# Kernel optimization log

Hardware: AMD Instinct MI355X
Metric: run time of the kernel (lower is better)

## Reference

```python
import jax, jax.numpy as jnp
import numpy as np

N, E, IN_DIM, HID, L = 50000, 800000, 64, 64, 3
EDGE_DIM = 2 * HID + 2  # src_h | dst_h | edge_feat


def setup_inputs() -> dict:
    key = jax.random.key(0)
    ks = jax.random.split(key, 32)
    s = 0.05
    inp = {
        "h": jax.random.normal(ks[0], (N, IN_DIM), jnp.float32),
        "e": jax.random.normal(ks[1], (E, 2), jnp.float32),
        "src": jax.random.randint(ks[2], (E,), 0, N),
        "dst": jax.random.randint(ks[3], (E,), 0, N),
        # input embedding
        "emb_W": jax.random.normal(ks[4], (IN_DIM, HID), jnp.float32) * s,
        "emb_b": jnp.zeros((HID,), jnp.float32),
        # per-GIN-layer params (stacked over L)
        "eps": jnp.zeros((L,), jnp.float32),  # learn_eps init 0
        "mlp_W1": jax.random.normal(ks[5], (L, HID, HID), jnp.float32) * s,
        "mlp_b1": jnp.zeros((L, HID), jnp.float32),
        "mlp_bn_s": jnp.ones((L, HID), jnp.float32),   # eval-mode BN folded: x*s+sh
        "mlp_bn_sh": jnp.zeros((L, HID), jnp.float32),
        "mlp_W2": jax.random.normal(ks[6], (L, HID, HID), jnp.float32) * s,
        "mlp_b2": jnp.zeros((L, HID), jnp.float32),
        "apply_bn_s": jnp.ones((L, HID), jnp.float32),
        "apply_bn_sh": jnp.zeros((L, HID), jnp.float32),
        "gin_bn_s": jnp.ones((L, HID), jnp.float32),
        "gin_bn_sh": jnp.zeros((L, HID), jnp.float32),
        # prediction heads (L+1 of them)
        "pred_W1": jax.random.normal(ks[7], (L + 1, EDGE_DIM, HID), jnp.float32) * s,
        "pred_b1": jnp.zeros((L + 1, HID), jnp.float32),
        "pred_W2": jax.random.normal(ks[8], (L + 1, HID, 1), jnp.float32) * s,
        "pred_b2": jnp.zeros((L + 1, 1), jnp.float32),
    }
    return inp


def reference(h, e, src, dst, emb_W, emb_b, eps,
              mlp_W1, mlp_b1, mlp_bn_s, mlp_bn_sh, mlp_W2, mlp_b2,
              apply_bn_s, apply_bn_sh, gin_bn_s, gin_bn_sh,
              pred_W1, pred_b1, pred_W2, pred_b2):
    n = h.shape[0]
    bn = lambda x, sc, sh: x * sc + sh  # eval-mode batchnorm (folded scale/shift)

    h = h @ emb_W + emb_b  # [N, HID]

    def edge_feat(hh):
        # gather node features onto edges: [E, 2*HID+2]
        return jnp.concatenate([hh[src], hh[dst], e], axis=1)

    def pred(ef, i):
        z = jax.nn.relu(ef @ pred_W1[i] + pred_b1[i])
        return z @ pred_W2[i] + pred_b2[i]  # [E, 1]

    score = pred(edge_feat(h), 0)
    for i in range(L):
        h_in = h
        # GIN sum aggregation: copy src features, sum at dst
        neigh = jax.ops.segment_sum(h[src], dst, num_segments=n)
        x = (1.0 + eps[i]) * h + neigh
        # MLP: Linear -> BN -> ReLU -> Linear
        x = jax.nn.relu(bn(x @ mlp_W1[i] + mlp_b1[i], mlp_bn_s[i], mlp_bn_sh[i]))
        x = x @ mlp_W2[i] + mlp_b2[i]
        # ApplyNodeFunc: BN -> ReLU
        x = jax.nn.relu(bn(x, apply_bn_s[i], apply_bn_sh[i]))
        # GINLayer post: BN -> ReLU -> residual (dropout=0 in eval)
        x = jax.nn.relu(bn(x, gin_bn_s[i], gin_bn_sh[i]))
        h = h_in + x
        score = score + pred(edge_feat(h), i + 1)
    return jax.nn.relu(score)
```

## Files before the change

### kernel.cpp

```cpp
#include <hip/hip_runtime.h>

typedef unsigned short ushort_t;
typedef unsigned int uint_t;

static __device__ __forceinline__ ushort_t f2bf(float f) {
    uint_t u = __float_as_uint(f);
    uint_t r = (u + 0x7FFFu + ((u >> 16) & 1u)) >> 16;
    return (ushort_t)r;
}
static __device__ __forceinline__ float bf2f(ushort_t u) {
    return __uint_as_float(((uint_t)u) << 16);
}
static __device__ __forceinline__ float bf2f_lo(uint_t u) {
    return __uint_as_float(u << 16);
}
static __device__ __forceinline__ float bf2f_hi(uint_t u) {
    return __uint_as_float(u & 0xffff0000u);
}
static __device__ __forceinline__ uint_t pack2(float lo, float hi) {
    return (uint_t)f2bf(lo) | ((uint_t)f2bf(hi) << 16);
}

static __device__ __forceinline__ float edge_p2(
    uint_t ax, uint_t ay, float4 brow, float ex, float ey,
    float4 wc0, float4 wc1, float4 w2v)
{
    float z0 = bf2f_lo(ax) + brow.x + ex*wc0.x + ey*wc1.x; z0 = fmaxf(z0, 0.f);
    float z1 = bf2f_hi(ax) + brow.y + ex*wc0.y + ey*wc1.y; z1 = fmaxf(z1, 0.f);
    float z2 = bf2f_lo(ay) + brow.z + ex*wc0.z + ey*wc1.z; z2 = fmaxf(z2, 0.f);
    float z3 = bf2f_hi(ay) + brow.w + ex*wc0.w + ey*wc1.w; z3 = fmaxf(z3, 0.f);
    return z0*w2v.x + z1*w2v.y + z2*w2v.z + z3*w2v.w;
}

#define RED16(p) { p += __shfl_xor(p,1); p += __shfl_xor(p,2); \
                   p += __shfl_xor(p,4); p += __shfl_xor(p,8); }

__global__ __launch_bounds__(256) void k_count(
    const int* __restrict__ dst, int* __restrict__ deg, int E)
{
    int e = blockIdx.x * 256 + threadIdx.x;
    if (e < E) atomicAdd(&deg[dst[e]], 1);
}

__global__ __launch_bounds__(1024) void k_scanA(
    const int* __restrict__ deg, int* __restrict__ partial,
    int* __restrict__ bsum, int N)
{
    __shared__ int wsum[16];
    int tid = threadIdx.x, lane = tid & 63, wid = tid >> 6;
    int idx = blockIdx.x * 1024 + tid;
    int v = (idx < N) ? deg[idx] : 0;
    int x = v;
#pragma unroll
    for (int o = 1; o < 64; o <<= 1) {
        int t = __shfl_up(x, o, 64);
        if (lane >= o) x += t;
    }
    if (lane == 63) wsum[wid] = x;
    __syncthreads();
    if (wid == 0) {
        int s = (lane < 16) ? wsum[lane] : 0;
#pragma unroll
        for (int o = 1; o < 16; o <<= 1) {
            int t = __shfl_up(s, o, 64);
            if (lane >= o) s += t;
        }
        if (lane < 16) wsum[lane] = s;
    }
    __syncthreads();
    int woff = (wid > 0) ? wsum[wid - 1] : 0;
    if (idx < N) partial[idx] = woff + x - v;
    if (tid == 0) bsum[blockIdx.x] = wsum[15];
}

__global__ __launch_bounds__(256) void k_scanB(
    int* __restrict__ bsum, int nb, int* __restrict__ totalp)
{
    __shared__ int s[256];
    int tid = threadIdx.x;
    int v = (tid < nb) ? bsum[tid] : 0;
    s[tid] = v;
    __syncthreads();
#pragma unroll
    for (int off = 1; off < 256; off <<= 1) {
        int t = (tid >= off) ? s[tid - off] : 0;
        __syncthreads();
        s[tid] += t;
        __syncthreads();
    }
    if (tid < nb) bsum[tid] = s[tid] - v;
    if (tid == 0) totalp[0] = s[255];
}

__global__ __launch_bounds__(256) void k_scanC(
    int* __restrict__ offsets, const int* __restrict__ bsum,
    int* __restrict__ cursor, int N)
{
    int idx = blockIdx.x * 256 + threadIdx.x;
    if (idx >= N) return;
    int o = offsets[idx] + bsum[idx >> 10];
    offsets[idx] = o;
    cursor[idx] = o;
}

__global__ __launch_bounds__(256) void k_fill(
    const int* __restrict__ src, const int* __restrict__ dst,
    const float* __restrict__ ep, int* __restrict__ cursor,
    int4* __restrict__ entries, int E)
{
    int ei = blockIdx.x * 256 + threadIdx.x;
    if (ei >= E) return;
    int pos = atomicAdd(&cursor[dst[ei]], 1);
    float2 ev = *(const float2*)(ep + 2 * (size_t)ei);
    entries[pos] = make_int4(src[ei], ei, __float_as_int(ev.x), __float_as_int(ev.y));
}

static __device__ __forceinline__ int deg_bucket(int d) {
    return d >= 63 ? 0 : (63 - d);
}

__global__ __launch_bounds__(256) void k_bcount(
    const int* __restrict__ offsets, int* __restrict__ bcnt, int N)
{
    __shared__ int hist[64];
    int tid = threadIdx.x;
    if (tid < 64) hist[tid] = 0;
    __syncthreads();
    int idx = blockIdx.x * 256 + tid;
    if (idx < N) {
        int d = offsets[idx + 1] - offsets[idx];
        atomicAdd(&hist[deg_bucket(d)], 1);
    }
    __syncthreads();
    if (tid < 64 && hist[tid]) atomicAdd(&bcnt[tid], hist[tid]);
}

__global__ __launch_bounds__(64) void k_bscan(
    int* __restrict__ bcnt, int* __restrict__ bcur)
{
    int lane = threadIdx.x;
    int v = bcnt[lane];
    int x = v;
#pragma unroll
    for (int o = 1; o < 64; o <<= 1) {
        int t = __shfl_up(x, o, 64);
        if (lane >= o) x += t;
    }
    bcur[lane] = x - v;
}

__global__ __launch_bounds__(256) void k_bfill(
    const int* __restrict__ offsets, int* __restrict__ bcur,
    int* __restrict__ perm, int N)
{
    __shared__ int hist[64];
    __shared__ int lbase[64];
    int tid = threadIdx.x;
    if (tid < 64) hist[tid] = 0;
    __syncthreads();
    int idx = blockIdx.x * 256 + tid;
    int b = 0, rank = 0;
    bool valid = (idx < N);
    if (valid) {
        int d = offsets[idx + 1] - offsets[idx];
        b = deg_bucket(d);
        rank = atomicAdd(&hist[b], 1);
    }
    __syncthreads();
    if (tid < 64) lbase[tid] = hist[tid] ? atomicAdd(&bcur[tid], hist[tid]) : 0;
    __syncthreads();
    if (valid) perm[lbase[b] + rank] = idx;
}

template <int WRITE>
static __device__ __forceinline__ void epi_tables16(
    float (*xs)[68], int row16, int li, int r, float4 o,
    const float* __restrict__ WAn, const float* __restrict__ bAn,
    const float* __restrict__ WBn,
    ushort_t* __restrict__ tab_out, ushort_t* __restrict__ B_out)
{
    xs[row16][4*li+0] = o.x; xs[row16][4*li+1] = o.y;
    xs[row16][4*li+2] = o.z; xs[row16][4*li+3] = o.w;
    float4 aA = *(const float4*)(bAn + 4 * li);
    float4 aB = make_float4(0.f, 0.f, 0.f, 0.f);
#pragma unroll
    for (int k = 0; k < 64; k++) {
        float xk = xs[row16][k];
        float4 wa = *(const float4*)(WAn + k * 64 + 4 * li);
        float4 wb = *(const float4*)(WBn + k * 64 + 4 * li);
        aA.x += xk * wa.x; aA.y += xk * wa.y; aA.z += xk * wa.z; aA.w += xk * wa.w;
        aB.x += xk * wb.x; aB.y += xk * wb.y; aB.z += xk * wb.z; aB.w += xk * wb.w;
    }
    if (WRITE == 1) {
        int4 cw;
        cw.x = (int)pack2(aA.x, aA.y);
        cw.y = (int)pack2(aA.z, aA.w);
        cw.z = (int)pack2(o.x, o.y);
        cw.w = (int)pack2(o.z, o.w);
        *(int4*)(tab_out + (size_t)r * 128 + li * 8) = cw;
    } else {
        ushort4 oa;
        oa.x = f2bf(aA.x); oa.y = f2bf(aA.y); oa.z = f2bf(aA.z); oa.w = f2bf(aA.w);
        *(ushort4*)(tab_out + (size_t)r * 64 + 4 * li) = oa;
    }
    ushort4 ob;
    ob.x = f2bf(aB.x); ob.y = f2bf(aB.y); ob.z = f2bf(aB.z); ob.w = f2bf(aB.w);
    *(ushort4*)(B_out + (size_t)r * 64 + 4 * li) = ob;
}

__global__ __launch_bounds__(256) void k_embed_ab(
    const float* __restrict__ in, const float* __restrict__ W,
    const float* __restrict__ bias, float* __restrict__ hout,
    const float* __restrict__ WA, const float* __restrict__ bA,
    const float* __restrict__ WB,
    ushort_t* __restrict__ comb_out, ushort_t* __restrict__ B_out, int N)
{
    __shared__ float xs[16][68];
    const int row16 = threadIdx.x >> 4;
    const int li    = threadIdx.x & 15;
    const int r     = blockIdx.x * 16 + row16;
    if (r >= N) return;
    float4 x4 = *(const float4*)(in + (size_t)r * 64 + 4 * li);
    xs[row16][4*li+0] = x4.x; xs[row16][4*li+1] = x4.y;
    xs[row16][4*li+2] = x4.z; xs[row16][4*li+3] = x4.w;
    float4 acc = *(const float4*)(bias + 4 * li);
#pragma unroll
    for (int k = 0; k < 64; k++) {
        float xk = xs[row16][k];
        float4 wv = *(const float4*)(W + k * 64 + 4 * li);
        acc.x += xk * wv.x; acc.y += xk * wv.y;
        acc.z += xk * wv.z; acc.w += xk * wv.w;
    }
    *(float4*)(hout + (size_t)r * 64 + 4 * li) = acc;
    epi_tables16<1>(xs, row16, li, r, acc, WA, bA, WB, comb_out, B_out);
}

__global__ __launch_bounds__(256) void k_tables(
    const float* __restrict__ h,
    const float* __restrict__ WA, const float* __restrict__ bA,
    const float* __restrict__ WB,
    ushort_t* __restrict__ comb_out, ushort_t* __restrict__ B_out, int N)
{
    __shared__ float xs[16][68];
    const int row16 = threadIdx.x >> 4;
    const int li    = threadIdx.x & 15;
    const int r     = blockIdx.x * 16 + row16;
    if (r >= N) return;
    float4 o = *(const float4*)(h + (size_t)r * 64 + 4 * li);
    epi_tables16<1>(xs, row16, li, r, o, WA, bA, WB, comb_out, B_out);
}

template <int MODE, int EPI>
__global__ __launch_bounds__(256) void k_fused(
    const float* __restrict__ h, float* __restrict__ hout,
    const ushort_t* __restrict__ comb, const ushort_t* __restrict__ Bm,
    const int4* __restrict__ entries, const int* __restrict__ offsets,
    const int* __restrict__ perm,
    float* __restrict__ score_csr,
    const float* __restrict__ Wc, const float* __restrict__ W2v,
    const float* __restrict__ b2p, const float* __restrict__ epsp,
    const float* __restrict__ W1, const float* __restrict__ b1,
    const float* __restrict__ s1, const float* __restrict__ sh1,
    const float* __restrict__ W2, const float* __restrict__ b2,
    const float* __restrict__ as_, const float* __restrict__ ash,
    const float* __restrict__ gs, const float* __restrict__ gsh,
    const float* __restrict__ WAn, const float* __restrict__ bAn,
    const float* __restrict__ WBn,
    ushort_t* __restrict__ tab_out, ushort_t* __restrict__ B_out, int N)
{
    __shared__ float xs[16][68];
    __shared__ float ts[16][68];
    const int row16 = threadIdx.x >> 4;
    const int li    = threadIdx.x & 15;
    const int idx   = blockIdx.x * 16 + row16;
    if (idx >= N) return;
    const int r = perm[idx];

    const float4 wc0 = *(const float4*)(Wc + li*4);
    const float4 wc1 = *(const float4*)(Wc + 64 + li*4);
    const float4 w2v = *(const float4*)(W2v + li*4);
    const float bb2 = b2p[0];
    ushort4 bu = *(const ushort4*)(Bm + (size_t)r * 64 + li*4);
    const float4 brow = make_float4(bf2f(bu.x), bf2f(bu.y), bf2f(bu.z), bf2f(bu.w));

    const int beg = offsets[r], end = offsets[r + 1];
    float4 acc = make_float4(0.f, 0.f, 0.f, 0.f);

    for (int k = beg; k < end; k += 8) {
        int4 ee[8];
#pragma unroll
        for (int j = 0; j < 8; j++) {
            int kj = k + j; kj = kj < end ? kj : end - 1;
            ee[j] = entries[kj];
        }
        int4 cc[8];
#pragma unroll
        for (int j = 0; j < 8; j++)
            cc[j] = *(const int4*)(comb + (size_t)ee[j].x * 128 + li * 8);
#pragma unroll
        for (int j = 0; j < 8; j++) {
            const bool ok = (k + j < end);
            uint_t hz = ok ? (uint_t)cc[j].z : 0u;
            uint_t hw = ok ? (uint_t)cc[j].w : 0u;
            acc.x += bf2f_lo(hz); acc.y += bf2f_hi(hz);
            acc.z += bf2f_lo(hw); acc.w += bf2f_hi(hw);
        }
#pragma unroll
        for (int j = 0; j < 8; j++) {
            float p = edge_p2((uint_t)cc[j].x, (uint_t)cc[j].y, brow,
                              __int_as_float(ee[j].z), __int_as_float(ee[j].w),
                              wc0, wc1, w2v);
            RED16(p)
            if (li == 0 && (k + j < end)) {
                if (MODE == 0) score_csr[k + j] = p + bb2;
                else           score_csr[k + j] += p + bb2;
            }
        }
    }

    const float epsv = 1.0f + epsp[0];
    float4 hv = *(const float4*)(h + (size_t)r * 64 + 4 * li);
    xs[row16][4*li+0] = epsv * hv.x + acc.x;
    xs[row16][4*li+1] = epsv * hv.y + acc.y;
    xs[row16][4*li+2] = epsv * hv.z + acc.z;
    xs[row16][4*li+3] = epsv * hv.w + acc.w;

    float4 t = *(const float4*)(b1 + 4 * li);
#pragma unroll
    for (int kk = 0; kk < 64; kk++) {
        float xk = xs[row16][kk];
        float4 wv = *(const float4*)(W1 + kk * 64 + 4 * li);
        t.x += xk * wv.x; t.y += xk * wv.y; t.z += xk * wv.z; t.w += xk * wv.w;
    }
    {
        float4 sc = *(const float4*)(s1 + 4 * li);
        float4 sh = *(const float4*)(sh1 + 4 * li);
        t.x = fmaxf(t.x * sc.x + sh.x, 0.f);
        t.y = fmaxf(t.y * sc.y + sh.y, 0.f);
        t.z = fmaxf(t.z * sc.z + sh.z, 0.f);
        t.w = fmaxf(t.w * sc.w + sh.w, 0.f);
    }
    ts[row16][4*li+0] = t.x; ts[row16][4*li+1] = t.y;
    ts[row16][4*li+2] = t.z; ts[row16][4*li+3] = t.w;

    float4 u = *(const float4*)(b2 + 4 * li);
#pragma unroll
    for (int kk = 0; kk < 64; kk++) {
        float tk = ts[row16][kk];
        float4 wv = *(const float4*)(W2 + kk * 64 + 4 * li);
        u.x += tk * wv.x; u.y += tk * wv.y; u.z += tk * wv.z; u.w += tk * wv.w;
    }
    {
        float4 sc = *(const float4*)(as_ + 4 * li);
        float4 sh = *(const float4*)(ash + 4 * li);
        u.x = fmaxf(u.x * sc.x + sh.x, 0.f);
        u.y = fmaxf(u.y * sc.y + sh.y, 0.f);
        u.z = fmaxf(u.z * sc.z + sh.z, 0.f);
        u.w = fmaxf(u.w * sc.w + sh.w, 0.f);
        sc = *(const float4*)(gs + 4 * li);
        sh = *(const float4*)(gsh + 4 * li);
        u.x = fmaxf(u.x * sc.x + sh.x, 0.f);
        u.y = fmaxf(u.y * sc.y + sh.y, 0.f);
        u.z = fmaxf(u.z * sc.z + sh.z, 0.f);
        u.w = fmaxf(u.w * sc.w + sh.w, 0.f);
    }
    float4 o = make_float4(hv.x + u.x, hv.y + u.y, hv.z + u.z, hv.w + u.w);
    *(float4*)(hout + (size_t)r * 64 + 4 * li) = o;

    if (EPI == 1)
        epi_tables16<1>(xs, row16, li, r, o, WAn, bAn, WBn, tab_out, B_out);
    else if (EPI == 2)
        epi_tables16<2>(xs, row16, li, r, o, WAn, bAn, WBn, tab_out, B_out);
}

template <int COMPACT>
__global__ __launch_bounds__(256) void k_head(
    const ushort_t* __restrict__ Atab,
    const ushort_t* __restrict__ Bm,
    const int4* __restrict__ entries, const int* __restrict__ offsets,
    const int* __restrict__ perm,
    const float* __restrict__ score_csr, float* __restrict__ score_out,
    const float* __restrict__ Wc, const float* __restrict__ W2v,
    const float* __restrict__ b2p, int N)
{
    const int row16 = threadIdx.x >> 4;
    const int li    = threadIdx.x & 15;
    const int idx   = blockIdx.x * 16 + row16;
    if (idx >= N) return;
    const int r = perm[idx];

    const float4 wc0 = *(const float4*)(Wc + li*4);
    const float4 wc1 = *(const float4*)(Wc + 64 + li*4);
    const float4 w2v = *(const float4*)(W2v + li*4);
    const float bb2 = b2p[0];
    ushort4 bu = *(const ushort4*)(Bm + (size_t)r * 64 + li*4);
    const float4 brow = make_float4(bf2f(bu.x), bf2f(bu.y), bf2f(bu.z), bf2f(bu.w));

    const int beg = offsets[r], end = offsets[r + 1];

    for (int k = beg; k < end; k += 8) {
        int4 ee[8];
#pragma unroll
        for (int j = 0; j < 8; j++) {
            int kj = k + j; kj = kj < end ? kj : end - 1;
            ee[j] = entries[kj];
        }
        uint_t ax[8], ay[8];
#pragma unroll
        for (int j = 0; j < 8; j++) {
            if (COMPACT) {
                ushort4 a = *(const ushort4*)(Atab + (size_t)ee[j].x * 64 + li * 4);
                ax[j] = (uint_t)a.x | ((uint_t)a.y << 16);
                ay[j] = (uint_t)a.z | ((uint_t)a.w << 16);
            } else {
                int2 d = *(const int2*)(Atab + (size_t)ee[j].x * 128 + li * 8);
                ax[j] = (uint_t)d.x; ay[j] = (uint_t)d.y;
            }
        }
#pragma unroll
        for (int j = 0; j < 8; j++) {
            float p = edge_p2(ax[j], ay[j], brow,
                              __int_as_float(ee[j].z), __int_as_float(ee[j].w),
                              wc0, wc1, w2v);
            RED16(p)
            if (li == 0 && (k + j < end))
                score_out[ee[j].y] = fmaxf(score_csr[k + j] + p + bb2, 0.f);
        }
    }
}

extern "C" void kernel_launch(void* const* d_in, const int* in_sizes, int n_in,
                              void* d_out, int out_size, void* d_ws, size_t ws_size,
                              hipStream_t stream) {
    const float* h_in  = (const float*)d_in[0];
    const float* e     = (const float*)d_in[1];
    const int*   src   = (const int*)d_in[2];
    const int*   dst   = (const int*)d_in[3];
    const float* emb_W = (const float*)d_in[4];
    const float* emb_b = (const float*)d_in[5];
    const float* eps   = (const float*)d_in[6];
    const float* mW1   = (const float*)d_in[7];
    const float* mb1   = (const float*)d_in[8];
    const float* mbs   = (const float*)d_in[9];
    const float* mbsh  = (const float*)d_in[10];
    const float* mW2   = (const float*)d_in[11];
    const float* mb2   = (const float*)d_in[12];
    const float* as_   = (const float*)d_in[13];
    const float* ash   = (const float*)d_in[14];
    const float* gs    = (const float*)d_in[15];
    const float* gsh   = (const float*)d_in[16];
    const float* pW1   = (const float*)d_in[17];
    const float* pb1   = (const float*)d_in[18];
    const float* pW2   = (const float*)d_in[19];
    const float* pb2   = (const float*)d_in[20];

    const int N  = in_sizes[0] / 64;
    const int E  = in_sizes[2];
    const int Lr = in_sizes[6];
    const size_t nrow = (size_t)N * 64;

    float* score = (float*)d_out;

    char* wp = (char*)d_ws;
    auto take = [&](size_t b) -> char* {
        char* p = wp; wp += (b + 255) & ~(size_t)255; return p;
    };
    float*    h0        = (float*)take(nrow * 4);
    float*    h1        = (float*)take(nrow * 4);
    ushort_t* comb0     = (ushort_t*)take(nrow * 4);
    ushort_t* B0        = (ushort_t*)take(nrow * 2);
    int4*     entries   = (int4*)take((size_t)E * 16);
    float*    score_csr = (float*)take((size_t)E * 4);
    int*      offsets   = (int*)take((size_t)(N + 1) * 4);
    int*      cursor    = (int*)take((size_t)N * 4);
    int*      bsum      = (int*)take(1024);
    int*      perm      = (int*)take((size_t)N * 4);
    int*      bcnt      = (int*)take(64 * 4);
    int*      bcur      = (int*)take(64 * 4);
    ushort_t* comb1     = (ushort_t*)take(nrow * 4);
    ushort_t* B1        = (ushort_t*)take(nrow * 2);
    ushort_t* Afin      = (ushort_t*)take(nrow * 2);
    size_t need_epi = (size_t)(wp - (char*)d_ws);

    const bool use_epi = ws_size >= need_epi;

    const int rowBlocks = (N + 15) / 16;
    const int edgeGrid  = (E + 255) / 256;
    const int nb        = (N + 1023) / 1024;

    hipMemsetAsync(cursor, 0, (size_t)N * sizeof(int), stream);
    k_count<<<edgeGrid, 256, 0, stream>>>(dst, cursor, E);
    k_scanA<<<nb, 1024, 0, stream>>>(cursor, offsets, bsum, N);
    k_scanB<<<1, 256, 0, stream>>>(bsum, nb, offsets + N);
    k_scanC<<<(N + 255) / 256, 256, 0, stream>>>(offsets, bsum, cursor, N);
    k_fill<<<edgeGrid, 256, 0, stream>>>(src, dst, e, cursor, entries, E);

    hipMemsetAsync(bcnt, 0, 64 * sizeof(int), stream);
    k_bcount<<<(N + 255) / 256, 256, 0, stream>>>(offsets, bcnt, N);
    k_bscan<<<1, 64, 0, stream>>>(bcnt, bcur);
    k_bfill<<<(N + 255) / 256, 256, 0, stream>>>(offsets, bcur, perm, N);

    k_embed_ab<<<rowBlocks, 256, 0, stream>>>(
        h_in, emb_W, emb_b, h0, pW1, pb1, pW1 + 64 * 64, comb0, B0, N);

    float* hcur = h0;       float* hnext = h1;
    ushort_t* Ccur = comb0; ushort_t* Cnxt = use_epi ? comb1 : comb0;
    ushort_t* Bcur = B0;    ushort_t* Bnxt = use_epi ? B1 : B0;

    for (int i = 0; i < Lr; i++) {
        const float* pw  = pW1 + (size_t)i * 130 * 64;
        const float* Wc  = pw + 128 * 64;
        const float* w2  = pW2 + (size_t)i * 64;
        const float* b2  = pb2 + i;
        const float* pwn = pW1 + (size_t)(i + 1) * 130 * 64;
        const float* gW1 = mW1 + (size_t)i * 64 * 64;
        const float* gW2 = mW2 + (size_t)i * 64 * 64;
        const bool last = (i == Lr - 1);

        if (use_epi) {
            ushort_t* tout = last ? Afin : Cnxt;
            if (i == 0 && !last)
                k_fused<0,1><<<rowBlocks, 256, 0, stream>>>(
                    hcur, hnext, Ccur, Bcur, entries, offsets, perm, score_csr,
                    Wc, w2, b2, eps + i,
                    gW1, mb1 + i*64, mbs + i*64, mbsh + i*64, gW2, mb2 + i*64,
                    as_ + i*64, ash + i*64, gs + i*64, gsh + i*64,
                    pwn, pb1 + (i+1)*64, pwn + 64*64, tout, Bnxt, N);
            else if (i == 0 && last)
                k_fused<0,2><<<rowBlocks, 256, 0, stream>>>(
                    hcur, hnext, Ccur, Bcur, entries, offsets, perm, score_csr,
                    Wc, w2, b2, eps + i,
                    gW1, mb1 + i*64, mbs + i*64, mbsh + i*64, gW2, mb2 + i*64,
                    as_ + i*64, ash + i*64, gs + i*64, gsh + i*64,
                    pwn, pb1 + (i+1)*64, pwn + 64*64, tout, Bnxt, N);
            else if (!last)
                k_fused<1,1><<<rowBlocks, 256, 0, stream>>>(
                    hcur, hnext, Ccur, Bcur, entries, offsets, perm, score_csr,
                    Wc, w2, b2, eps + i,
                    gW1, mb1 + i*64, mbs + i*64, mbsh + i*64, gW2, mb2 + i*64,
                    as_ + i*64, ash + i*64, gs + i*64, gsh + i*64,
                    pwn, pb1 + (i+1)*64, pwn + 64*64, tout, Bnxt, N);
            else
                k_fused<1,2><<<rowBlocks, 256, 0, stream>>>(
                    hcur, hnext, Ccur, Bcur, entries, offsets, perm, score_csr,
                    Wc, w2, b2, eps + i,
                    gW1, mb1 + i*64, mbs + i*64, mbsh + i*64, gW2, mb2 + i*64,
                    as_ + i*64, ash + i*64, gs + i*64, gsh + i*64,
                    pwn, pb1 + (i+1)*64, pwn + 64*64, tout, Bnxt, N);
            { ushort_t* t = Ccur; Ccur = Cnxt; Cnxt = t; }
            { ushort_t* t = Bcur; Bcur = Bnxt; Bnxt = t; }
        } else {
            if (i == 0)
                k_fused<0,0><<<rowBlocks, 256, 0, stream>>>(
                    hcur, hnext, Ccur, Bcur, entries, offsets, perm, score_csr,
                    Wc, w2, b2, eps + i,
                    gW1, mb1 + i*64, mbs + i*64, mbsh + i*64, gW2, mb2 + i*64,
                    as_ + i*64, ash + i*64, gs + i*64, gsh + i*64,
                    nullptr, nullptr, nullptr, nullptr, nullptr, N);
            else
                k_fused<1,0><<<rowBlocks, 256, 0, stream>>>(
                    hcur, hnext, Ccur, Bcur, entries, offsets, perm, score_csr,
                    Wc, w2, b2, eps + i,
                    gW1, mb1 + i*64, mbs + i*64, mbsh + i*64, gW2, mb2 + i*64,
                    as_ + i*64, ash + i*64, gs + i*64, gsh + i*64,
                    nullptr, nullptr, nullptr, nullptr, nullptr, N);
            k_tables<<<rowBlocks, 256, 0, stream>>>(
                hnext, pwn, pb1 + (i+1)*64, pwn + 64*64, Ccur, Bcur, N);
        }
        { float* t = hcur; hcur = hnext; hnext = t; }
    }

    {
        const float* pw = pW1 + (size_t)Lr * 130 * 64;
        const float* Wc = pw + 128 * 64;
        const float* w2 = pW2 + (size_t)Lr * 64;
        const float* b2 = pb2 + Lr;
        if (use_epi)
            k_head<1><<<rowBlocks, 256, 0, stream>>>(
                Afin, Bcur, entries, offsets, perm, score_csr, score,
                Wc, w2, b2, N);
        else
            k_head<0><<<rowBlocks, 256, 0, stream>>>(
                Ccur, Bcur, entries, offsets, perm, score_csr, score,
                Wc, w2, b2, N);
    }
}
```

Measured before the change: 612.9 us.

## Fuse degree histogram into scan, unroll edge loops by four with exact tails

Computes the degree-bucket histogram inside the scan kernel from the raw degree counts, which removes the separate k_bcount launch and its re-read of offsets. Replaces the padded 8-wide edge batches in the fused aggregation and final scoring kernels with 4-wide unrolled loops plus a scalar tail, so low-degree nodes no longer do clamped duplicate loads and masked work. It also reuses one shared-memory tile instead of two. The trade-off is less memory-level parallelism per iteration for high-degree nodes and duplicated code for the tail loop.

```diff
diff --git a/kernel.cpp b/kernel.cpp
--- a/kernel.cpp
+++ b/kernel.cpp
@@ -42,14 +42,22 @@
     if (e < E) atomicAdd(&deg[dst[e]], 1);
 }
 
+static __device__ __forceinline__ int deg_bucket(int d) {
+    return d >= 63 ? 0 : (63 - d);
+}
+
 __global__ __launch_bounds__(1024) void k_scanA(
     const int* __restrict__ deg, int* __restrict__ partial,
-    int* __restrict__ bsum, int N)
+    int* __restrict__ bsum, int* __restrict__ bcnt, int N)
 {
     __shared__ int wsum[16];
+    __shared__ int hist[64];
     int tid = threadIdx.x, lane = tid & 63, wid = tid >> 6;
+    if (tid < 64) hist[tid] = 0;
+    __syncthreads();
     int idx = blockIdx.x * 1024 + tid;
     int v = (idx < N) ? deg[idx] : 0;
+    if (idx < N) atomicAdd(&hist[deg_bucket(v)], 1);
     int x = v;
 #pragma unroll
     for (int o = 1; o < 64; o <<= 1) {
@@ -71,6 +79,8 @@
     int woff = (wid > 0) ? wsum[wid - 1] : 0;
     if (idx < N) partial[idx] = woff + x - v;
     if (tid == 0) bsum[blockIdx.x] = wsum[15];
+    __syncthreads();
+    if (tid < 64 && hist[tid]) atomicAdd(&bcnt[tid], hist[tid]);
 }
 
 __global__ __launch_bounds__(256) void k_scanB(
@@ -113,26 +123,6 @@
     int pos = atomicAdd(&cursor[dst[ei]], 1);
     float2 ev = *(const float2*)(ep + 2 * (size_t)ei);
     entries[pos] = make_int4(src[ei], ei, __float_as_int(ev.x), __float_as_int(ev.y));
-}
-
-static __device__ __forceinline__ int deg_bucket(int d) {
-    return d >= 63 ? 0 : (63 - d);
-}
-
-__global__ __launch_bounds__(256) void k_bcount(
-    const int* __restrict__ offsets, int* __restrict__ bcnt, int N)
-{
-    __shared__ int hist[64];
-    int tid = threadIdx.x;
-    if (tid < 64) hist[tid] = 0;
-    __syncthreads();
-    int idx = blockIdx.x * 256 + tid;
-    if (idx < N) {
-        int d = offsets[idx + 1] - offsets[idx];
-        atomicAdd(&hist[deg_bucket(d)], 1);
-    }
-    __syncthreads();
-    if (tid < 64 && hist[tid]) atomicAdd(&bcnt[tid], hist[tid]);
 }
 
 __global__ __launch_bounds__(64) void k_bscan(
@@ -174,18 +164,18 @@
 
 template <int WRITE>
 static __device__ __forceinline__ void epi_tables16(
-    float (*xs)[68], int row16, int li, int r, float4 o,
+    float (*xs)[68], int row, int li, int r, float4 o,
     const float* __restrict__ WAn, const float* __restrict__ bAn,
     const float* __restrict__ WBn,
     ushort_t* __restrict__ tab_out, ushort_t* __restrict__ B_out)
 {
-    xs[row16][4*li+0] = o.x; xs[row16][4*li+1] = o.y;
-    xs[row16][4*li+2] = o.z; xs[row16][4*li+3] = o.w;
+    xs[row][4*li+0] = o.x; xs[row][4*li+1] = o.y;
+    xs[row][4*li+2] = o.z; xs[row][4*li+3] = o.w;
     float4 aA = *(const float4*)(bAn + 4 * li);
     float4 aB = make_float4(0.f, 0.f, 0.f, 0.f);
 #pragma unroll
     for (int k = 0; k < 64; k++) {
-        float xk = xs[row16][k];
+        float xk = xs[row][k];
         float4 wa = *(const float4*)(WAn + k * 64 + 4 * li);
         float4 wb = *(const float4*)(WBn + k * 64 + 4 * li);
         aA.x += xk * wa.x; aA.y += xk * wa.y; aA.z += xk * wa.z; aA.w += xk * wa.w;
@@ -269,7 +259,6 @@
     ushort_t* __restrict__ tab_out, ushort_t* __restrict__ B_out, int N)
 {
     __shared__ float xs[16][68];
-    __shared__ float ts[16][68];
     const int row16 = threadIdx.x >> 4;
     const int li    = threadIdx.x & 15;
     const int idx   = blockIdx.x * 16 + row16;
@@ -286,35 +275,47 @@
     const int beg = offsets[r], end = offsets[r + 1];
     float4 acc = make_float4(0.f, 0.f, 0.f, 0.f);
 
-    for (int k = beg; k < end; k += 8) {
-        int4 ee[8];
-#pragma unroll
-        for (int j = 0; j < 8; j++) {
-            int kj = k + j; kj = kj < end ? kj : end - 1;
-            ee[j] = entries[kj];
+    int k = beg;
+    for (; k + 3 < end; k += 4) {
+        int4 e0 = entries[k], e1 = entries[k+1], e2 = entries[k+2], e3 = entries[k+3];
+        int4 c0 = *(const int4*)(comb + (size_t)e0.x * 128 + li * 8);
+        int4 c1 = *(const int4*)(comb + (size_t)e1.x * 128 + li * 8);
+        int4 c2 = *(const int4*)(comb + (size_t)e2.x * 128 + li * 8);
+        int4 c3 = *(const int4*)(comb + (size_t)e3.x * 128 + li * 8);
+        acc.x += bf2f_lo(c0.z) + bf2f_lo(c1.z) + bf2f_lo(c2.z) + bf2f_lo(c3.z);
+        acc.y += bf2f_hi(c0.z) + bf2f_hi(c1.z) + bf2f_hi(c2.z) + bf2f_hi(c3.z);
+        acc.z += bf2f_lo(c0.w) + bf2f_lo(c1.w) + bf2f_lo(c2.w) + bf2f_lo(c3.w);
+        acc.w += bf2f_hi(c0.w) + bf2f_hi(c1.w) + bf2f_hi(c2.w) + bf2f_hi(c3.w);
+        float p0 = edge_p2((uint_t)c0.x, (uint_t)c0.y, brow,
+                           __int_as_float(e0.z), __int_as_float(e0.w), wc0, wc1, w2v);
+        float p1 = edge_p2((uint_t)c1.x, (uint_t)c1.y, brow,
+                           __int_as_float(e1.z), __int_as_float(e1.w), wc0, wc1, w2v);
+        float p2 = edge_p2((uint_t)c2.x, (uint_t)c2.y, brow,
+                           __int_as_float(e2.z), __int_as_float(e2.w), wc0, wc1, w2v);
+        float p3 = edge_p2((uint_t)c3.x, (uint_t)c3.y, brow,
+                           __int_as_float(e3.z), __int_as_float(e3.w), wc0, wc1, w2v);
+        RED16(p0) RED16(p1) RED16(p2) RED16(p3)
+        if (li == 0) {
+            if (MODE == 0) {
+                score_csr[k]   = p0 + bb2; score_csr[k+1] = p1 + bb2;
+                score_csr[k+2] = p2 + bb2; score_csr[k+3] = p3 + bb2;
+            } else {
+                score_csr[k]   += p0 + bb2; score_csr[k+1] += p1 + bb2;
+                score_csr[k+2] += p2 + bb2; score_csr[k+3] += p3 + bb2;
+            }
         }
-        int4 cc[8];
-#pragma unroll
-        for (int j = 0; j < 8; j++)
-            cc[j] = *(const int4*)(comb + (size_t)ee[j].x * 128 + li * 8);
-#pragma unroll
-        for (int j = 0; j < 8; j++) {
-            const bool ok = (k + j < end);
-            uint_t hz = ok ? (uint_t)cc[j].z : 0u;
-            uint_t hw = ok ? (uint_t)cc[j].w : 0u;
-            acc.x += bf2f_lo(hz); acc.y += bf2f_hi(hz);
-            acc.z += bf2f_lo(hw); acc.w += bf2f_hi(hw);
-        }
-#pragma unroll
-        for (int j = 0; j < 8; j++) {
-            float p = edge_p2((uint_t)cc[j].x, (uint_t)cc[j].y, brow,
-                              __int_as_float(ee[j].z), __int_as_float(ee[j].w),
-                              wc0, wc1, w2v);
-            RED16(p)
-            if (li == 0 && (k + j < end)) {
-                if (MODE == 0) score_csr[k + j] = p + bb2;
-                else           score_csr[k + j] += p + bb2;
-            }
+    }
+    for (; k < end; k++) {
+        int4 e0 = entries[k];
+        int4 c0 = *(const int4*)(comb + (size_t)e0.x * 128 + li * 8);
+        acc.x += bf2f_lo((uint_t)c0.z); acc.y += bf2f_hi((uint_t)c0.z);
+        acc.z += bf2f_lo((uint_t)c0.w); acc.w += bf2f_hi((uint_t)c0.w);
+        float p0 = edge_p2((uint_t)c0.x, (uint_t)c0.y, brow,
+                           __int_as_float(e0.z), __int_as_float(e0.w), wc0, wc1, w2v);
+        RED16(p0)
+        if (li == 0) {
+            if (MODE == 0) score_csr[k] = p0 + bb2;
+            else           score_csr[k] += p0 + bb2;
         }
     }
 
@@ -340,13 +341,13 @@
         t.z = fmaxf(t.z * sc.z + sh.z, 0.f);
         t.w = fmaxf(t.w * sc.w + sh.w, 0.f);
     }
-    ts[row16][4*li+0] = t.x; ts[row16][4*li+1] = t.y;
-    ts[row16][4*li+2] = t.z; ts[row16][4*li+3] = t.w;
+    xs[row16][4*li+0] = t.x; xs[row16][4*li+1] = t.y;
+    xs[row16][4*li+2] = t.z; xs[row16][4*li+3] = t.w;
 
     float4 u = *(const float4*)(b2 + 4 * li);
 #pragma unroll
     for (int kk = 0; kk < 64; kk++) {
-        float tk = ts[row16][kk];
+        float tk = xs[row16][kk];
         float4 wv = *(const float4*)(W2 + kk * 64 + 4 * li);
         u.x += tk * wv.x; u.y += tk * wv.y; u.z += tk * wv.z; u.w += tk * wv.w;
     }
@@ -398,35 +399,38 @@
 
     const int beg = offsets[r], end = offsets[r + 1];
 
-    for (int k = beg; k < end; k += 8) {
-        int4 ee[8];
-#pragma unroll
-        for (int j = 0; j < 8; j++) {
-            int kj = k + j; kj = kj < end ? kj : end - 1;
-            ee[j] = entries[kj];
-        }
-        uint_t ax[8], ay[8];
-#pragma unroll
-        for (int j = 0; j < 8; j++) {
-            if (COMPACT) {
-                ushort4 a = *(const ushort4*)(Atab + (size_t)ee[j].x * 64 + li * 4);
-                ax[j] = (uint_t)a.x | ((uint_t)a.y << 16);
-                ay[j] = (uint_t)a.z | ((uint_t)a.w << 16);
-            } else {
-                int2 d = *(const int2*)(Atab + (size_t)ee[j].x * 128 + li * 8);
-                ax[j] = (uint_t)d.x; ay[j] = (uint_t)d.y;
-            }
-        }
-#pragma unroll
-        for (int j = 0; j < 8; j++) {
-            float p = edge_p2(ax[j], ay[j], brow,
-                              __int_as_float(ee[j].z), __int_as_float(ee[j].w),
-                              wc0, wc1, w2v);
-            RED16(p)
-            if (li == 0 && (k + j < end))
-                score_out[ee[j].y] = fmaxf(score_csr[k + j] + p + bb2, 0.f);
-        }
-    }
+#define ALOAD(s, ax, ay) { \
+    if (COMPACT) { \
+        ushort4 a_ = *(const ushort4*)(Atab + (size_t)(s) * 64 + li * 4); \
+        ax = (uint_t)a_.x | ((uint_t)a_.y << 16); \
+        ay = (uint_t)a_.z | ((uint_t)a_.w << 16); \
+    } else { \
+        int2 d_ = *(const int2*)(Atab + (size_t)(s) * 128 + li * 8); \
+        ax = (uint_t)d_.x; ay = (uint_t)d_.y; \
+    } }
+#define HSCOR(kk, e_, ax, ay) { \
+    float p_ = edge_p2(ax, ay, brow, __int_as_float((e_).z), __int_as_float((e_).w), \
+                       wc0, wc1, w2v); \
+    RED16(p_) \
+    if (li == 0) score_out[(e_).y] = fmaxf(score_csr[kk] + p_ + bb2, 0.f); }
+
+    int k = beg;
+    for (; k + 3 < end; k += 4) {
+        int4 e0 = entries[k], e1 = entries[k+1], e2 = entries[k+2], e3 = entries[k+3];
+        uint_t ax0, ay0, ax1, ay1, ax2, ay2, ax3, ay3;
+        ALOAD(e0.x, ax0, ay0) ALOAD(e1.x, ax1, ay1)
+        ALOAD(e2.x, ax2, ay2) ALOAD(e3.x, ax3, ay3)
+        HSCOR(k, e0, ax0, ay0) HSCOR(k+1, e1, ax1, ay1)
+        HSCOR(k+2, e2, ax2, ay2) HSCOR(k+3, e3, ax3, ay3)
+    }
+    for (; k < end; k++) {
+        int4 e0 = entries[k];
+        uint_t ax0, ay0;
+        ALOAD(e0.x, ax0, ay0)
+        HSCOR(k, e0, ax0, ay0)
+    }
+#undef ALOAD
+#undef HSCOR
 }
 
 extern "C" void kernel_launch(void* const* d_in, const int* in_sizes, int n_in,
@@ -489,14 +493,13 @@
     const int nb        = (N + 1023) / 1024;
 
     hipMemsetAsync(cursor, 0, (size_t)N * sizeof(int), stream);
+    hipMemsetAsync(bcnt, 0, 64 * sizeof(int), stream);
     k_count<<<edgeGrid, 256, 0, stream>>>(dst, cursor, E);
-    k_scanA<<<nb, 1024, 0, stream>>>(cursor, offsets, bsum, N);
+    k_scanA<<<nb, 1024, 0, stream>>>(cursor, offsets, bsum, bcnt, N);
     k_scanB<<<1, 256, 0, stream>>>(bsum, nb, offsets + N);
     k_scanC<<<(N + 255) / 256, 256, 0, stream>>>(offsets, bsum, cursor, N);
     k_fill<<<edgeGrid, 256, 0, stream>>>(src, dst, e, cursor, entries, E);
 
-    hipMemsetAsync(bcnt, 0, 64 * sizeof(int), stream);
-    k_bcount<<<(N + 255) / 256, 256, 0, stream>>>(offsets, bcnt, N);
     k_bscan<<<1, 64, 0, stream>>>(bcnt, bcur);
     k_bfill<<<(N + 255) / 256, 256, 0, stream>>>(offsets, bcur, perm, N);
 
```

New measurement: 587.8 us. -4.1%, faster.
